# Optimization experiments

Measured on AMD Instinct MI355X. Metric: run time of the kernel, lower is better.

The kernel has to match this reference:

```python
import jax, jax.numpy as jnp
import numpy as np

B, T, C, H, HD = 2, 2048, 768, 12, 64


def setup_inputs() -> dict:
    key = jax.random.key(0)
    k0, k1, k2, k3 = jax.random.split(key, 4)
    x = jax.random.normal(k0, (B, T, C), dtype=jnp.float32)
    w_attn = jax.random.normal(k1, (3 * H * HD, C), dtype=jnp.float32) * 0.02
    b_attn = jnp.zeros((3 * H * HD,), dtype=jnp.float32)
    w_proj = jax.random.normal(k2, (C, H * HD), dtype=jnp.float32) * 0.02
    b_proj = jnp.zeros((C,), dtype=jnp.float32)
    sel_w = jax.random.normal(k3, (H,), dtype=jnp.float32) * 0.3
    return {"x": x, "w_attn": w_attn, "b_attn": b_attn,
            "w_proj": w_proj, "b_proj": b_proj, "sel_w": sel_w}


def reference(x, w_attn, b_attn, w_proj, b_proj, sel_w):
    Bc, Tc, Cc = x.shape
    Hc = sel_w.shape[0]
    HDc = w_attn.shape[0] // (3 * Hc)
    qkv = x @ w_attn.T + b_attn                          # [B,T,3*H*HD]
    q, k, v = jnp.split(qkv, 3, axis=2)
    q = q.reshape(Bc, Tc, Hc, HDc).transpose(0, 2, 1, 3)  # [B,H,T,HD]
    k = k.reshape(Bc, Tc, Hc, HDc).transpose(0, 2, 1, 3)
    v = v.reshape(Bc, Tc, Hc, HDc).transpose(0, 2, 1, 3)

    scale = 1.0 / np.sqrt(HDc).astype(np.float32)
    att = jnp.einsum('bhid,bhjd->bhij', q, k) * scale    # [B,H,T,T]
    causal = jnp.tril(jnp.ones((Tc, Tc), dtype=bool))
    neg_inf = jnp.asarray(-jnp.inf, dtype=att.dtype)
    att = jnp.where(causal[None, None], att, neg_inf)

    # selection head: per-head linear combo of (causally-zeroed) logits
    att0 = jnp.where(causal[None, None], att, 0.0)       # -inf -> 0 before combo
    S = jnp.einsum('bhij,h->bij', att0, sel_w)           # [B,T,T], bias=False
    S = jnp.where(causal[None], S, 0.0)
    S = jax.nn.relu(S)
    S = S.at[..., 0].set(0.0)                            # protect_bos_token
    S = S * (1.0 - jnp.eye(Tc, dtype=S.dtype))           # prevent_from_masking_myself

    FF = jnp.cumsum(S, axis=-2)                          # forgetting accumulation over rows
    FF_shifted = jnp.concatenate(
        [jnp.zeros_like(FF[..., :1, :]), FF[..., :-1, :]], axis=-2)

    att = jax.nn.softmax(att - FF_shifted[:, None], axis=-1)
    y = jnp.einsum('bhij,bhjd->bhid', att, v)            # [B,H,T,HD]
    y = y.transpose(0, 2, 1, 3).reshape(Bc, Tc, Hc * HDc)
    return y @ w_proj.T + b_proj
```

## Files before the change

### kernel.cpp

```cpp
#include <hip/hip_runtime.h>

#define B_   2
#define T_   2048
#define C_   768
#define H_   12
#define HD_  64
#define M_   (B_ * T_)
#define N3_  (3 * C_)
#define KB_  (C_ * 2)

typedef __bf16 bf16_t;
typedef bf16_t bf16x8 __attribute__((ext_vector_type(8)));
typedef float  floatx4 __attribute__((ext_vector_type(4)));

__device__ inline floatx4 mfma_bf16(bf16x8 a, bf16x8 b, floatx4 c) {
    return __builtin_amdgcn_mfma_f32_16x16x32_bf16(a, b, c, 0, 0, 0);
}

__device__ __forceinline__ void async_copy16(const void* g, void* l) {
    __builtin_amdgcn_global_load_lds(
        (const __attribute__((address_space(1))) void*)g,
        (__attribute__((address_space(3))) void*)l, 16, 0, 0);
}

__device__ __forceinline__ void stage8k(const char* tile, char* ldsbase,
                                        int k0b, int wave, int lane) {
#pragma unroll
    for (int i = 0; i < 2; ++i) {
        int p = (wave * 2 + i) * 64 + lane;
        int r = p >> 2, slot = p & 3;
        int g = slot ^ ((r >> 1) & 3);
        async_copy16(tile + (size_t)r * KB_ + k0b + g * 16, ldsbase + p * 16);
    }
}

__device__ __forceinline__ bf16x8 frag_read(const char* ldsbase, int row, int quad) {
    int slot = quad ^ ((row >> 1) & 3);
    return *(const bf16x8*)(ldsbase + row * 64 + slot * 16);
}

template<bool TRIPLE>
__device__ __forceinline__ void gemm_loop(
    const char* Ah, const char* Al, const char* Bh, const char* Bl,
    char* lds, floatx4 (&acc)[4][4])
{
    int tid = threadIdx.x, lane = tid & 63, wave = tid >> 6;
    int l15 = lane & 15, quad = lane >> 4;
    int wr = wave >> 1, wc = wave & 1;
    char* LAh = lds;
    char* LAl = lds + 8192;
    char* LBh = lds + (TRIPLE ? 16384 : 8192);
    char* LBl = lds + 24576;
#pragma unroll 1
    for (int k0 = 0; k0 < KB_; k0 += 64) {
        __syncthreads();
        stage8k(Ah, LAh, k0, wave, lane);
        if (TRIPLE) stage8k(Al, LAl, k0, wave, lane);
        stage8k(Bh, LBh, k0, wave, lane);
        if (TRIPLE) stage8k(Bl, LBl, k0, wave, lane);
        __syncthreads();
        bf16x8 ah[4], al[4], bh[4], bl[4];
#pragma unroll
        for (int t = 0; t < 4; ++t) {
            ah[t] = frag_read(LAh, wr * 64 + t * 16 + l15, quad);
            bh[t] = frag_read(LBh, wc * 64 + t * 16 + l15, quad);
            if (TRIPLE) {
                al[t] = frag_read(LAl, wr * 64 + t * 16 + l15, quad);
                bl[t] = frag_read(LBl, wc * 64 + t * 16 + l15, quad);
            }
        }
#pragma unroll
        for (int mi = 0; mi < 4; ++mi)
#pragma unroll
            for (int ni = 0; ni < 4; ++ni) {
                acc[mi][ni] = mfma_bf16(ah[mi], bh[ni], acc[mi][ni]);
                if (TRIPLE) {
                    acc[mi][ni] = mfma_bf16(ah[mi], bl[ni], acc[mi][ni]);
                    acc[mi][ni] = mfma_bf16(al[mi], bh[ni], acc[mi][ni]);
                }
            }
    }
}

__global__ __launch_bounds__(256) void split_f32(
    const float* __restrict__ src, bf16_t* __restrict__ hi,
    bf16_t* __restrict__ lo, int n)
{
    int i = blockIdx.x * 256 + threadIdx.x;
    if (i < n) {
        float f = src[i];
        bf16_t h = (bf16_t)f;
        hi[i] = h;
        lo[i] = (bf16_t)(f - (float)h);
    }
}

__global__ __launch_bounds__(256) void conv_f32(
    const float* __restrict__ src, bf16_t* __restrict__ dst, int n)
{
    int i = blockIdx.x * 256 + threadIdx.x;
    if (i < n) dst[i] = (bf16_t)src[i];
}

__global__ __launch_bounds__(256) void qkv_gemm(
    const bf16_t* __restrict__ x_hi, const bf16_t* __restrict__ x_lo,
    const bf16_t* __restrict__ w_hi, const bf16_t* __restrict__ w_lo,
    const float* __restrict__ bias, const float* __restrict__ selw,
    bf16_t* __restrict__ q_hi, bf16_t* __restrict__ q_lo,
    bf16_t* __restrict__ kw_hi, bf16_t* __restrict__ kw_lo,
    bf16_t* __restrict__ k_b, bf16_t* __restrict__ v_b)
{
    extern __shared__ char lds[];
    int m0 = blockIdx.x * 128, n0 = blockIdx.y * 128;
    floatx4 acc[4][4];
#pragma unroll
    for (int i = 0; i < 4; ++i)
#pragma unroll
        for (int j = 0; j < 4; ++j) acc[i][j] = (floatx4){0.f, 0.f, 0.f, 0.f};
    if (n0 >= 2 * C_) {
        gemm_loop<false>((const char*)(x_hi + (size_t)m0 * C_), nullptr,
                         (const char*)(w_hi + (size_t)n0 * C_), nullptr, lds, acc);
    } else {
        gemm_loop<true>((const char*)(x_hi + (size_t)m0 * C_),
                        (const char*)(x_lo + (size_t)m0 * C_),
                        (const char*)(w_hi + (size_t)n0 * C_),
                        (const char*)(w_lo + (size_t)n0 * C_), lds, acc);
    }

    int tid = threadIdx.x, lane = tid & 63, wave = tid >> 6;
    int l15 = lane & 15, quad = lane >> 4;
    int wr = wave >> 1, wc = wave & 1;
    int cb = n0 + wc * 64;
#pragma unroll
    for (int ni = 0; ni < 4; ++ni) {
        int col = cb + ni * 16 + l15;
        float bb = bias[col];
#pragma unroll
        for (int mi = 0; mi < 4; ++mi)
#pragma unroll
            for (int r = 0; r < 4; ++r) {
                int row = m0 + wr * 64 + mi * 16 + quad * 4 + r;
                float v = acc[mi][ni][r] + bb;
                if (cb < C_) {
                    float vs = v * 0.125f;
                    bf16_t h = (bf16_t)vs;
                    q_hi[(size_t)row * C_ + col] = h;
                    q_lo[(size_t)row * C_ + col] = (bf16_t)(vs - (float)h);
                } else if (cb < 2 * C_) {
                    int c2 = col - C_;
                    k_b[(size_t)row * C_ + c2] = (bf16_t)v;
                    float kw = v * selw[c2 >> 6];
                    bf16_t h = (bf16_t)kw;
                    kw_hi[(size_t)row * C_ + c2] = h;
                    kw_lo[(size_t)row * C_ + c2] = (bf16_t)(kw - (float)h);
                } else {
                    v_b[(size_t)row * C_ + (col - 2 * C_)] = (bf16_t)v;
                }
            }
    }
}

__global__ __launch_bounds__(256) void s_gemm(
    const bf16_t* __restrict__ q_hi, const bf16_t* __restrict__ q_lo,
    const bf16_t* __restrict__ kw_hi, const bf16_t* __restrict__ kw_lo,
    float* __restrict__ SF)
{
    extern __shared__ char lds[];
    int i0 = blockIdx.x * 128, j0 = blockIdx.y * 128, b = blockIdx.z;
    float* out = SF + (size_t)b * T_ * T_;
    int tid = threadIdx.x;
    if (j0 > i0) {
        float4 z = {0.f, 0.f, 0.f, 0.f};
        float* p = out + (size_t)(i0 + (tid >> 1)) * T_ + j0 + (tid & 1) * 64;
#pragma unroll
        for (int c = 0; c < 16; ++c) ((float4*)p)[c] = z;
        return;
    }
    floatx4 acc[4][4];
#pragma unroll
    for (int i = 0; i < 4; ++i)
#pragma unroll
        for (int j = 0; j < 4; ++j) acc[i][j] = (floatx4){0.f, 0.f, 0.f, 0.f};
    size_t arow = ((size_t)b * T_ + i0) * C_;
    size_t brow = ((size_t)b * T_ + j0) * C_;
    gemm_loop<true>((const char*)(q_hi + arow), (const char*)(q_lo + arow),
                    (const char*)(kw_hi + brow), (const char*)(kw_lo + brow),
                    lds, acc);

    int lane = tid & 63, wave = tid >> 6;
    int l15 = lane & 15, quad = lane >> 4;
    int wr = wave >> 1, wc = wave & 1;
#pragma unroll
    for (int ni = 0; ni < 4; ++ni) {
        int j = j0 + wc * 64 + ni * 16 + l15;
#pragma unroll
        for (int mi = 0; mi < 4; ++mi)
#pragma unroll
            for (int r = 0; r < 4; ++r) {
                int i = i0 + wr * 64 + mi * 16 + quad * 4 + r;
                float s = acc[mi][ni][r];
                s = (j >= 1 && j < i) ? fmaxf(s, 0.f) : 0.f;
                out[(size_t)i * T_ + j] = s;
            }
    }
}

#define SEG_    16
#define SEGLEN_ (T_ / SEG_)

__global__ __launch_bounds__(256) void scan_seg_sum(
    const float* __restrict__ SF, float* __restrict__ segsum)
{
    int gid  = blockIdx.x * 256 + threadIdx.x;
    int j    = gid & (T_ - 1);
    int rest = gid >> 11;
    int seg  = rest & (SEG_ - 1);
    int b    = rest >> 4;
    const float* col = SF + (size_t)b * T_ * T_ + (size_t)(seg * SEGLEN_) * T_ + j;
    float s = 0.f;
#pragma unroll 8
    for (int i = 0; i < SEGLEN_; ++i) s += col[(size_t)i * T_];
    segsum[((size_t)b * SEG_ + seg) * T_ + j] = s;
}

__global__ __launch_bounds__(256) void scan_seg_excl(float* __restrict__ segsum)
{
    int gid = blockIdx.x * 256 + threadIdx.x;
    int j = gid & (T_ - 1);
    int b = gid >> 11;
    float run = 0.f;
#pragma unroll
    for (int s = 0; s < SEG_; ++s) {
        size_t idx = ((size_t)b * SEG_ + s) * T_ + j;
        float v = segsum[idx];
        segsum[idx] = run;
        run += v;
    }
}

__global__ __launch_bounds__(256) void scan_apply(
    float* __restrict__ SF, const float* __restrict__ segsum)
{
    int gid  = blockIdx.x * 256 + threadIdx.x;
    int j    = gid & (T_ - 1);
    int rest = gid >> 11;
    int seg  = rest & (SEG_ - 1);
    int b    = rest >> 4;
    float run = segsum[((size_t)b * SEG_ + seg) * T_ + j];
    float* col = SF + (size_t)b * T_ * T_ + (size_t)(seg * SEGLEN_) * T_ + j;
#pragma unroll 4
    for (int i = 0; i < SEGLEN_; ++i) {
        float s = col[(size_t)i * T_];
        col[(size_t)i * T_] = run;
        run += s;
    }
}

__global__ __launch_bounds__(256) void vt_kernel(
    const bf16_t* __restrict__ v_b, bf16_t* __restrict__ vt)
{
    __shared__ bf16_t tile[64][72];
    int t0 = blockIdx.x * 64, h = blockIdx.y, b = blockIdx.z;
    int tid = threadIdx.x;
    int r = tid >> 2, sl = tid & 3;
    const bf16_t* src = v_b + ((size_t)(b * T_ + t0 + r)) * C_ + h * HD_ + sl * 16;
    *(int4*)&tile[r][sl * 16]     = *(const int4*)src;
    *(int4*)&tile[r][sl * 16 + 8] = *(const int4*)(src + 8);
    __syncthreads();
    int hd = tid >> 2, q = tid & 3;
#pragma unroll
    for (int half = 0; half < 2; ++half) {
        int c0 = (q * 2 + half) * 8;
        union { int4 i4; bf16_t e[8]; } u;
#pragma unroll
        for (int kk = 0; kk < 8; ++kk) u.e[kk] = tile[c0 + kk][hd];
        *(int4*)(vt + ((size_t)(b * H_ + h) * HD_ + hd) * T_ + t0 + c0) = u.i4;
    }
}

__global__ __launch_bounds__(256) void attn_kernel(
    const bf16_t* __restrict__ q_b, const bf16_t* __restrict__ k_b,
    const bf16_t* __restrict__ vt_g, const float* __restrict__ FF,
    bf16_t* __restrict__ y_b)
{
    __shared__ __align__(16) char KL[2][8192];
    __shared__ __align__(16) char VL[2][8192];
    __shared__ __align__(16) float LS[4][16][68];

    int tid = threadIdx.x, lane = tid & 63, wave = tid >> 6;
    int l15 = lane & 15, quad = lane >> 4;
    int bi = (int)gridDim.x - 1 - (int)blockIdx.x;
    int h = blockIdx.y, b = blockIdx.z;
    int i0w = bi * 64 + wave * 16;
    int jmax = bi * 64 + 63;
    const floatx4 fzero = {0.f, 0.f, 0.f, 0.f};

    const bf16_t* qrow = q_b + ((size_t)b * T_ + i0w + l15) * C_ + h * HD_;
    bf16x8 qa0 = *(const bf16x8*)(qrow + quad * 8);
    bf16x8 qa1 = *(const bf16x8*)(qrow + 32 + quad * 8);

    const bf16_t* kbase = k_b + (size_t)b * T_ * C_ + h * HD_;
    const bf16_t* vbase = vt_g + (size_t)(b * H_ + h) * HD_ * T_;
    const float*  fp    = FF + ((size_t)b * T_ + i0w + l15) * T_ + quad * 8;

    auto stage = [&](int ph, int j0) {
#pragma unroll
        for (int i = 0; i < 2; ++i) {
            int p = (wave * 2 + i) * 64 + lane;
            int r = p >> 3, sp = p & 7, s = sp ^ (r & 7);
            async_copy16(kbase + (size_t)(j0 + r) * C_ + s * 8, &KL[ph][p * 16]);
        }
#pragma unroll
        for (int i = 0; i < 2; ++i) {
            int p = (wave * 2 + i) * 64 + lane;
            int r = p >> 3, sp = p & 7, s = sp ^ (r & 7);
            async_copy16(vbase + (size_t)r * T_ + j0 + s * 8, &VL[ph][p * 16]);
        }
    };

    float m_run = -__builtin_inff(), l_run = 0.f;
    floatx4 O[4];
#pragma unroll
    for (int nt = 0; nt < 4; ++nt) O[nt] = fzero;

    stage(0, 0);
    int ph = 0;
#pragma unroll 1
    for (int j0 = 0; j0 <= jmax; j0 += 64) {
        __syncthreads();
        if (j0 + 64 <= jmax) stage(ph ^ 1, j0 + 64);

        float ffv[16];
        *(floatx4*)&ffv[0]  = *(const floatx4*)(fp);
        *(floatx4*)&ffv[4]  = *(const floatx4*)(fp + 4);
        *(floatx4*)&ffv[8]  = *(const floatx4*)(fp + 32);
        *(floatx4*)&ffv[12] = *(const floatx4*)(fp + 36);
        fp += 64;

        floatx4 pc[4];
#pragma unroll
        for (int s = 0; s < 4; ++s) {
            int r = s * 16 + l15;
            bf16x8 k0 = *(const bf16x8*)&KL[ph][r * 128 + ((quad     ^ (r & 7)) * 16)];
            bf16x8 k1 = *(const bf16x8*)&KL[ph][r * 128 + (((quad+4) ^ (r & 7)) * 16)];
            floatx4 p = mfma_bf16(qa0, k0, fzero);
            pc[s] = mfma_bf16(qa1, k1, p);
        }
#pragma unroll
        for (int s = 0; s < 4; ++s)
#pragma unroll
            for (int r = 0; r < 4; ++r)
                LS[wave][quad * 4 + r][s * 16 + l15] = pc[s][r];
        float qk[16];
        *(floatx4*)&qk[0]  = *(const floatx4*)&LS[wave][l15][quad * 8];
        *(floatx4*)&qk[4]  = *(const floatx4*)&LS[wave][l15][quad * 8 + 4];
        *(floatx4*)&qk[8]  = *(const floatx4*)&LS[wave][l15][32 + quad * 8];
        *(floatx4*)&qk[12] = *(const floatx4*)&LS[wave][l15][32 + quad * 8 + 4];

        float lg[16];
#pragma unroll
        for (int c = 0; c < 16; ++c) lg[c] = qk[c] - ffv[c];
        if (j0 + 63 > i0w) {
            int i = i0w + l15;
#pragma unroll
            for (int c = 0; c < 16; ++c) {
                int j = j0 + (c >> 3) * 32 + quad * 8 + (c & 7);
                lg[c] = (j <= i) ? lg[c] : -__builtin_inff();
            }
        }
        float rm = lg[0];
#pragma unroll
        for (int c = 1; c < 16; ++c) rm = fmaxf(rm, lg[c]);
        rm = fmaxf(rm, __shfl_xor(rm, 16));
        rm = fmaxf(rm, __shfl_xor(rm, 32));
        float mn = fmaxf(m_run, rm);
        float mnu = fmaxf(mn, -1e30f);
        float alpha = __expf(m_run - mnu);
        float p[16], ps = 0.f;
#pragma unroll
        for (int c = 0; c < 16; ++c) { p[c] = __expf(lg[c] - mnu); ps += p[c]; }
        ps += __shfl_xor(ps, 16);
        ps += __shfl_xor(ps, 32);
        l_run = l_run * alpha + ps;
        m_run = mn;
#pragma unroll
        for (int r = 0; r < 4; ++r) {
            float ar = __shfl(alpha, quad * 4 + r);
#pragma unroll
            for (int nt = 0; nt < 4; ++nt) O[nt][r] *= ar;
        }
        bf16x8 pa0, pa1;
#pragma unroll
        for (int c = 0; c < 8; ++c) { pa0[c] = (bf16_t)p[c]; pa1[c] = (bf16_t)p[8 + c]; }
#pragma unroll
        for (int nt = 0; nt < 4; ++nt) {
            int r = nt * 16 + l15;
            bf16x8 v0 = *(const bf16x8*)&VL[ph][r * 128 + ((quad     ^ (r & 7)) * 16)];
            bf16x8 v1 = *(const bf16x8*)&VL[ph][r * 128 + (((quad+4) ^ (r & 7)) * 16)];
            O[nt] = mfma_bf16(pa0, v0, O[nt]);
            O[nt] = mfma_bf16(pa1, v1, O[nt]);
        }
        ph ^= 1;
    }

#pragma unroll
    for (int r = 0; r < 4; ++r) {
        float inv = 1.f / __shfl(l_run, quad * 4 + r);
        int i = i0w + quad * 4 + r;
#pragma unroll
        for (int nt = 0; nt < 4; ++nt)
            y_b[((size_t)b * T_ + i) * C_ + h * HD_ + nt * 16 + l15] =
                (bf16_t)(O[nt][r] * inv);
    }
}

__global__ __launch_bounds__(256) void proj_gemm(
    const bf16_t* __restrict__ y_b, const bf16_t* __restrict__ wp_b,
    const float* __restrict__ bias, float* __restrict__ out)
{
    extern __shared__ char lds[];
    int m0 = blockIdx.x * 128, n0 = blockIdx.y * 128;
    floatx4 acc[4][4];
#pragma unroll
    for (int i = 0; i < 4; ++i)
#pragma unroll
        for (int j = 0; j < 4; ++j) acc[i][j] = (floatx4){0.f, 0.f, 0.f, 0.f};
    gemm_loop<false>((const char*)(y_b + (size_t)m0 * C_), nullptr,
                     (const char*)(wp_b + (size_t)n0 * C_), nullptr, lds, acc);

    int tid = threadIdx.x, lane = tid & 63, wave = tid >> 6;
    int l15 = lane & 15, quad = lane >> 4;
    int wr = wave >> 1, wc = wave & 1;
#pragma unroll
    for (int ni = 0; ni < 4; ++ni) {
        int col = n0 + wc * 64 + ni * 16 + l15;
        float bb = bias[col];
#pragma unroll
        for (int mi = 0; mi < 4; ++mi)
#pragma unroll
            for (int r = 0; r < 4; ++r)
                out[(size_t)(m0 + wr * 64 + mi * 16 + quad * 4 + r) * C_ + col] =
                    acc[mi][ni][r] + bb;
    }
}

extern "C" void kernel_launch(void* const* d_in, const int* in_sizes, int n_in,
                              void* d_out, int out_size, void* d_ws, size_t ws_size,
                              hipStream_t stream)
{
    const float* x      = (const float*)d_in[0];
    const float* w_attn = (const float*)d_in[1];
    const float* b_attn = (const float*)d_in[2];
    const float* w_proj = (const float*)d_in[3];
    const float* b_proj = (const float*)d_in[4];
    const float* sel_w  = (const float*)d_in[5];
    float* out = (float*)d_out;

    char* ws = (char*)d_ws;
    size_t off = 0;
    auto alloc = [&](size_t bytes) {
        void* p = ws + off;
        off += (bytes + 255) & ~(size_t)255;
        return p;
    };
    const size_t MC2 = (size_t)M_ * C_ * 2;
    bf16_t* q_hi   = (bf16_t*)alloc(MC2);
    bf16_t* q_lo   = (bf16_t*)alloc(MC2);
    bf16_t* kw_hi  = (bf16_t*)alloc(MC2);
    bf16_t* kw_lo  = (bf16_t*)alloc(MC2);
    bf16_t* k_b    = (bf16_t*)alloc(MC2);
    bf16_t* v_b    = (bf16_t*)alloc(MC2);
    bf16_t* y_b    = (bf16_t*)alloc(MC2);
    bf16_t* wp_b   = (bf16_t*)alloc((size_t)C_ * C_ * 2);
    float*  segsum = (float*)alloc((size_t)B_ * SEG_ * T_ * 4);
    char* shared_base = (char*)alloc((size_t)B_ * T_ * T_ * 4);
    bf16_t* x_hi = (bf16_t*)shared_base;
    bf16_t* x_lo = (bf16_t*)(shared_base + MC2);
    bf16_t* w_hi = (bf16_t*)(shared_base + 2 * MC2);
    bf16_t* w_lo = (bf16_t*)(shared_base + 2 * MC2 + (size_t)N3_ * C_ * 2);
    float*  SF   = (float*)shared_base;
    bf16_t* vt   = kw_hi;

    int nx = M_ * C_, nw = N3_ * C_, np = C_ * C_;
    split_f32<<<dim3((nx + 255) / 256), 256, 0, stream>>>(x, x_hi, x_lo, nx);
    split_f32<<<dim3((nw + 255) / 256), 256, 0, stream>>>(w_attn, w_hi, w_lo, nw);
    conv_f32<<<dim3((np + 255) / 256), 256, 0, stream>>>(w_proj, wp_b, np);

    qkv_gemm<<<dim3(M_ / 128, N3_ / 128), 256, 32768, stream>>>(
        x_hi, x_lo, w_hi, w_lo, b_attn, sel_w,
        q_hi, q_lo, kw_hi, kw_lo, k_b, v_b);
    s_gemm<<<dim3(T_ / 128, T_ / 128, B_), 256, 32768, stream>>>(
        q_hi, q_lo, kw_hi, kw_lo, SF);
    vt_kernel<<<dim3(T_ / 64, H_, B_), 256, 0, stream>>>(v_b, vt);
    scan_seg_sum<<<dim3(B_ * SEG_ * T_ / 256), 256, 0, stream>>>(SF, segsum);
    scan_seg_excl<<<dim3(B_ * T_ / 256), 256, 0, stream>>>(segsum);
    scan_apply<<<dim3(B_ * SEG_ * T_ / 256), 256, 0, stream>>>(SF, segsum);
    attn_kernel<<<dim3(T_ / 64, H_, B_), 256, 0, stream>>>(q_hi, k_b, vt, SF, y_b);
    proj_gemm<<<dim3(M_ / 128, C_ / 128), 256, 16384, stream>>>(y_b, wp_b, b_proj, out);
}
```

Measured before the change: 306.5 us.

## Double-buffer GEMM LDS staging and fuse segment column sums into S GEMM

```diff
diff --git a/kernel.cpp b/kernel.cpp
--- a/kernel.cpp
+++ b/kernel.cpp
@@ -47,26 +47,31 @@
     int tid = threadIdx.x, lane = tid & 63, wave = tid >> 6;
     int l15 = lane & 15, quad = lane >> 4;
     int wr = wave >> 1, wc = wave & 1;
-    char* LAh = lds;
-    char* LAl = lds + 8192;
-    char* LBh = lds + (TRIPLE ? 16384 : 8192);
-    char* LBl = lds + 24576;
+    const int PH = TRIPLE ? 32768 : 16384;
+    auto stage = [&](int ph, int k0) {
+        char* base = lds + ph * PH;
+        stage8k(Ah, base, k0, wave, lane);
+        stage8k(Bh, base + 8192, k0, wave, lane);
+        if (TRIPLE) {
+            stage8k(Al, base + 16384, k0, wave, lane);
+            stage8k(Bl, base + 24576, k0, wave, lane);
+        }
+    };
+    stage(0, 0);
+    int ph = 0;
 #pragma unroll 1
     for (int k0 = 0; k0 < KB_; k0 += 64) {
         __syncthreads();
-        stage8k(Ah, LAh, k0, wave, lane);
-        if (TRIPLE) stage8k(Al, LAl, k0, wave, lane);
-        stage8k(Bh, LBh, k0, wave, lane);
-        if (TRIPLE) stage8k(Bl, LBl, k0, wave, lane);
-        __syncthreads();
+        if (k0 + 64 < KB_) stage(ph ^ 1, k0 + 64);
+        char* base = lds + ph * PH;
         bf16x8 ah[4], al[4], bh[4], bl[4];
 #pragma unroll
         for (int t = 0; t < 4; ++t) {
-            ah[t] = frag_read(LAh, wr * 64 + t * 16 + l15, quad);
-            bh[t] = frag_read(LBh, wc * 64 + t * 16 + l15, quad);
+            ah[t] = frag_read(base,         wr * 64 + t * 16 + l15, quad);
+            bh[t] = frag_read(base + 8192,  wc * 64 + t * 16 + l15, quad);
             if (TRIPLE) {
-                al[t] = frag_read(LAl, wr * 64 + t * 16 + l15, quad);
-                bl[t] = frag_read(LBl, wc * 64 + t * 16 + l15, quad);
+                al[t] = frag_read(base + 16384, wr * 64 + t * 16 + l15, quad);
+                bl[t] = frag_read(base + 24576, wc * 64 + t * 16 + l15, quad);
             }
         }
 #pragma unroll
@@ -79,6 +84,7 @@
                     acc[mi][ni] = mfma_bf16(al[mi], bh[ni], acc[mi][ni]);
                 }
             }
+        ph ^= 1;
     }
 }
 
@@ -160,22 +166,23 @@
     }
 }
 
+#define SEG_    16
+#define SEGLEN_ (T_ / SEG_)
+
 __global__ __launch_bounds__(256) void s_gemm(
     const bf16_t* __restrict__ q_hi, const bf16_t* __restrict__ q_lo,
     const bf16_t* __restrict__ kw_hi, const bf16_t* __restrict__ kw_lo,
-    float* __restrict__ SF)
+    float* __restrict__ SF, float* __restrict__ segsum)
 {
     extern __shared__ char lds[];
-    int i0 = blockIdx.x * 128, j0 = blockIdx.y * 128, b = blockIdx.z;
+    int t = blockIdx.x, b = blockIdx.z;
+    int it = (int)((sqrtf(8.f * t + 1.f) - 1.f) * 0.5f);
+    while ((it + 1) * (it + 2) / 2 <= t) ++it;
+    while (it * (it + 1) / 2 > t) --it;
+    int jt = t - it * (it + 1) / 2;
+    int i0 = it * 128, j0 = jt * 128;
     float* out = SF + (size_t)b * T_ * T_;
-    int tid = threadIdx.x;
-    if (j0 > i0) {
-        float4 z = {0.f, 0.f, 0.f, 0.f};
-        float* p = out + (size_t)(i0 + (tid >> 1)) * T_ + j0 + (tid & 1) * 64;
-#pragma unroll
-        for (int c = 0; c < 16; ++c) ((float4*)p)[c] = z;
-        return;
-    }
+
     floatx4 acc[4][4];
 #pragma unroll
     for (int i = 0; i < 4; ++i)
@@ -187,9 +194,10 @@
                     (const char*)(kw_hi + brow), (const char*)(kw_lo + brow),
                     lds, acc);
 
-    int lane = tid & 63, wave = tid >> 6;
+    int tid = threadIdx.x, lane = tid & 63, wave = tid >> 6;
     int l15 = lane & 15, quad = lane >> 4;
     int wr = wave >> 1, wc = wave & 1;
+    float colsum[4] = {0.f, 0.f, 0.f, 0.f};
 #pragma unroll
     for (int ni = 0; ni < 4; ++ni) {
         int j = j0 + wc * 64 + ni * 16 + l15;
@@ -201,56 +209,57 @@
                 float s = acc[mi][ni][r];
                 s = (j >= 1 && j < i) ? fmaxf(s, 0.f) : 0.f;
                 out[(size_t)i * T_ + j] = s;
+                colsum[ni] += s;
             }
     }
-}
-
-#define SEG_    16
-#define SEGLEN_ (T_ / SEG_)
-
-__global__ __launch_bounds__(256) void scan_seg_sum(
-    const float* __restrict__ SF, float* __restrict__ segsum)
+#pragma unroll
+    for (int ni = 0; ni < 4; ++ni) {
+        colsum[ni] += __shfl_xor(colsum[ni], 16);
+        colsum[ni] += __shfl_xor(colsum[ni], 32);
+    }
+    float* red = (float*)lds;
+    if (quad == 0) {
+#pragma unroll
+        for (int ni = 0; ni < 4; ++ni)
+            red[wr * 128 + wc * 64 + ni * 16 + l15] = colsum[ni];
+    }
+    __syncthreads();
+    if (wave < 2) {
+        float ssum = red[wave * 64 + lane] + red[128 + wave * 64 + lane];
+        segsum[((size_t)b * SEG_ + it) * T_ + j0 + wave * 64 + lane] = ssum;
+    }
+}
+
+__global__ __launch_bounds__(256) void scan_seg_excl(float* __restrict__ segsum)
+{
+    int gid = blockIdx.x * 256 + threadIdx.x;
+    int j = gid & (T_ - 1);
+    int b = gid >> 11;
+    float run = 0.f;
+#pragma unroll
+    for (int s = 0; s < SEG_; ++s) {
+        size_t idx = ((size_t)b * SEG_ + s) * T_ + j;
+        float v = (s * SEGLEN_ + SEGLEN_ - 1 <= j) ? 0.f : segsum[idx];
+        segsum[idx] = run;
+        run += v;
+    }
+}
+
+__global__ __launch_bounds__(256) void scan_apply(
+    float* __restrict__ SF, const float* __restrict__ segsum)
 {
     int gid  = blockIdx.x * 256 + threadIdx.x;
     int j    = gid & (T_ - 1);
     int rest = gid >> 11;
     int seg  = rest & (SEG_ - 1);
     int b    = rest >> 4;
-    const float* col = SF + (size_t)b * T_ * T_ + (size_t)(seg * SEGLEN_) * T_ + j;
-    float s = 0.f;
-#pragma unroll 8
-    for (int i = 0; i < SEGLEN_; ++i) s += col[(size_t)i * T_];
-    segsum[((size_t)b * SEG_ + seg) * T_ + j] = s;
-}
-
-__global__ __launch_bounds__(256) void scan_seg_excl(float* __restrict__ segsum)
-{
-    int gid = blockIdx.x * 256 + threadIdx.x;
-    int j = gid & (T_ - 1);
-    int b = gid >> 11;
-    float run = 0.f;
-#pragma unroll
-    for (int s = 0; s < SEG_; ++s) {
-        size_t idx = ((size_t)b * SEG_ + s) * T_ + j;
-        float v = segsum[idx];
-        segsum[idx] = run;
-        run += v;
-    }
-}
-
-__global__ __launch_bounds__(256) void scan_apply(
-    float* __restrict__ SF, const float* __restrict__ segsum)
-{
-    int gid  = blockIdx.x * 256 + threadIdx.x;
-    int j    = gid & (T_ - 1);
-    int rest = gid >> 11;
-    int seg  = rest & (SEG_ - 1);
-    int b    = rest >> 4;
+    if (seg * SEGLEN_ + SEGLEN_ - 1 < j) return;
     float run = segsum[((size_t)b * SEG_ + seg) * T_ + j];
     float* col = SF + (size_t)b * T_ * T_ + (size_t)(seg * SEGLEN_) * T_ + j;
 #pragma unroll 4
     for (int i = 0; i < SEGLEN_; ++i) {
         float s = col[(size_t)i * T_];
+        s = (seg * SEGLEN_ + i > j) ? s : 0.f;
         col[(size_t)i * T_] = run;
         run += s;
     }
@@ -486,15 +495,14 @@
     split_f32<<<dim3((nw + 255) / 256), 256, 0, stream>>>(w_attn, w_hi, w_lo, nw);
     conv_f32<<<dim3((np + 255) / 256), 256, 0, stream>>>(w_proj, wp_b, np);
 
-    qkv_gemm<<<dim3(M_ / 128, N3_ / 128), 256, 32768, stream>>>(
+    qkv_gemm<<<dim3(M_ / 128, N3_ / 128), 256, 65536, stream>>>(
         x_hi, x_lo, w_hi, w_lo, b_attn, sel_w,
         q_hi, q_lo, kw_hi, kw_lo, k_b, v_b);
-    s_gemm<<<dim3(T_ / 128, T_ / 128, B_), 256, 32768, stream>>>(
-        q_hi, q_lo, kw_hi, kw_lo, SF);
+    s_gemm<<<dim3(136, 1, B_), 256, 65536, stream>>>(
+        q_hi, q_lo, kw_hi, kw_lo, SF, segsum);
     vt_kernel<<<dim3(T_ / 64, H_, B_), 256, 0, stream>>>(v_b, vt);
-    scan_seg_sum<<<dim3(B_ * SEG_ * T_ / 256), 256, 0, stream>>>(SF, segsum);
     scan_seg_excl<<<dim3(B_ * T_ / 256), 256, 0, stream>>>(segsum);
     scan_apply<<<dim3(B_ * SEG_ * T_ / 256), 256, 0, stream>>>(SF, segsum);
     attn_kernel<<<dim3(T_ / 64, H_, B_), 256, 0, stream>>>(q_hi, k_b, vt, SF, y_b);
-    proj_gemm<<<dim3(M_ / 128, C_ / 128), 256, 16384, stream>>>(y_b, wp_b, b_proj, out);
-}
+    proj_gemm<<<dim3(M_ / 128, C_ / 128), 256, 32768, stream>>>(y_b, wp_b, b_proj, out);
+}
```

Result: faster. 282.1 us (-8.0%).
